# Optimization experiments

Measured on AMD Instinct MI355X. Metric: run time of the kernel, lower is better.

## Reference

```python
import jax, jax.numpy as jnp
import numpy as np

B, N, INP = 16, 1024, 256
HEADS, DIM_HEAD = 8, 32
INNER = HEADS * DIM_HEAD  # 256
OUP = 256
IH = IW = 32  # IH*IW == N


def _relative_index(ih, iw):
    # mirrors the torch __init__ construction (meshgrid indexing='ij')
    coords = np.stack(np.meshgrid(np.arange(ih), np.arange(iw), indexing='ij')).reshape(2, -1)
    rel = coords[:, :, None] - coords[:, None, :]  # [2, N, N]
    rel[0] += ih - 1
    rel[1] += iw - 1
    rel[0] *= 2 * iw - 1
    return rel.sum(0).reshape(-1)  # [N*N]


def setup_inputs() -> dict:
    key = jax.random.key(0)
    kx, kqkv, kout, kbias = jax.random.split(key, 4)
    x = jax.random.normal(kx, (B, N, INP), dtype=jnp.float32)
    w_qkv = jax.random.normal(kqkv, (INP, 3 * INNER), dtype=jnp.float32) * 0.02
    w_out = jax.random.normal(kout, (INNER, OUP), dtype=jnp.float32) * 0.02
    b_out = jnp.zeros((OUP,), dtype=jnp.float32)
    bias_table = jax.random.normal(kbias, ((2 * IH - 1) * (2 * IW - 1), HEADS), dtype=jnp.float32) * 0.02
    relative_index = jnp.asarray(_relative_index(IH, IW), dtype=jnp.int32)
    return {"x": x, "w_qkv": w_qkv, "w_out": w_out, "b_out": b_out,
            "bias_table": bias_table, "relative_index": relative_index}


def reference(x, w_qkv, w_out, b_out, bias_table, relative_index):
    b, n, _ = x.shape
    scale = DIM_HEAD ** (-0.5)
    qkv = x @ w_qkv  # [b, n, 3*inner]
    q, k, v = jnp.split(qkv, 3, axis=-1)
    split_heads = lambda t: t.reshape(b, n, HEADS, DIM_HEAD).transpose(0, 2, 1, 3)  # b h n d
    q, k, v = split_heads(q), split_heads(k), split_heads(v)
    dots = jnp.einsum('bhnd,bhmd->bhnm', q, k) * scale  # [b, h, n, n]
    # gather bias: (n*n, heads) -> (1, heads, n, n), matching '(h w) c -> 1 c h w'
    rel_bias = bias_table[relative_index].reshape(n, n, HEADS).transpose(2, 0, 1)[None]
    attn = jax.nn.softmax(dots + rel_bias, axis=-1)
    out = jnp.einsum('bhnm,bhmd->bhnd', attn, v)
    out = out.transpose(0, 2, 1, 3).reshape(b, n, INNER)  # b n (h d)
    return out @ w_out + b_out
```

## Files before the change

### kernel.cpp

```cpp
#include <hip/hip_runtime.h>
#include <hip/hip_bf16.h>

typedef __bf16 bf16;
typedef bf16 bf16x4 __attribute__((ext_vector_type(4)));
typedef bf16 bf16x8 __attribute__((ext_vector_type(8)));
typedef short s16x4 __attribute__((ext_vector_type(4)));
typedef float f32x4 __attribute__((ext_vector_type(4)));

#define MFMA32(A, B, C) __builtin_amdgcn_mfma_f32_16x16x32_bf16(A, B, C, 0, 0, 0)
#define MFMA16(A, B, C) __builtin_amdgcn_mfma_f32_16x16x16bf16_1k(A, B, C, 0, 0, 0)
#define GL2LDS16(gp, lp)                                                            \
  __builtin_amdgcn_global_load_lds((const __attribute__((address_space(1))) unsigned int*)(gp), \
                                   (__attribute__((address_space(3))) unsigned int*)(lp), 16, 0, 0)

static constexpr float SCALE = 0.17677669529663687f;
static constexpr float LOG2E = 1.4426950408889634f;

__global__ __launch_bounds__(256) void k_prep(const float* __restrict__ x,
                                              const float* __restrict__ wqkv,
                                              const float* __restrict__ wout,
                                              const float* __restrict__ table,
                                              const int* __restrict__ ridx,
                                              bf16* __restrict__ xb, bf16* __restrict__ wtq,
                                              bf16* __restrict__ wto, bf16* __restrict__ rbb) {
  const int tid = threadIdx.x;
  const int blk = blockIdx.x;
  if (blk < 2048) {
    int t = blk * 256 + tid;
    const float4* s = reinterpret_cast<const float4*>(x) + (size_t)t * 2;
    float4 a = s[0], c = s[1];
    bf16x8 o;
    o[0] = (bf16)a.x; o[1] = (bf16)a.y; o[2] = (bf16)a.z; o[3] = (bf16)a.w;
    o[4] = (bf16)c.x; o[5] = (bf16)c.y; o[6] = (bf16)c.z; o[7] = (bf16)c.w;
    reinterpret_cast<bf16x8*>(xb)[t] = o;
  } else if (blk < 3072) {
    int t = (blk - 2048) * 256 + tid;
    if (t < 196608) {
      int n = t >> 8, k = t & 255;
      wtq[t] = (bf16)wqkv[k * 768 + n];
    } else {
      int t2 = t - 196608;
      int n = t2 >> 8, k = t2 & 255;
      wto[t2] = (bf16)wout[k * 256 + n];
    }
  } else {
    const int bb2 = blk - 3072;
    const int qt = bb2 >> 6, kt = bb2 & 63;
    const int r = tid & 3, lane = tid >> 2;
    const int ln = lane & 15, quad = lane >> 4;
    const int qrow = qt * 16 + ln;
    const int key = kt * 16 + quad * 4 + r;
    const int idx = ridx[qrow * 1024 + key];
    const float4* p = reinterpret_cast<const float4*>(table) + idx * 2;
    float4 a = p[0], c = p[1];
    float vals[8] = {a.x, a.y, a.z, a.w, c.x, c.y, c.z, c.w};
    const int base = bb2 * 256 + tid;
#pragma unroll
    for (int h = 0; h < 8; ++h) rbb[h * 1048576 + base] = (bf16)(vals[h] * LOG2E);
  }
}

template <int EPI>
__global__ __launch_bounds__(256) void k_gemm(const bf16* __restrict__ A,
                                              const bf16* __restrict__ Bt,
                                              bf16* __restrict__ q, bf16* __restrict__ kk,
                                              bf16* __restrict__ vt, float* __restrict__ out,
                                              const float* __restrict__ bout) {
  __shared__ __align__(16) bf16 SM[16896];
  bf16(*As)[4096] = reinterpret_cast<bf16(*)[4096]>(SM);
  bf16(*Bs)[4096] = reinterpret_cast<bf16(*)[4096]>(SM + 8192);
  const int tid = threadIdx.x;
  const int ln = tid & 15, quad = (tid >> 4) & 3, wv = tid >> 6;
  const int wm = (wv >> 1) * 64, wn = (wv & 1) * 64;
  const int m0 = blockIdx.x * 128, n0 = blockIdx.y * 128;
  const int srow = tid >> 2, scg = (tid & 3) * 8;
  const bf16* ag = A + (size_t)(m0 + srow) * 256 + scg;
  const bf16* bg = Bt + (size_t)(n0 + srow) * 256 + scg;
  f32x4 acc[4][4] = {};

  GL2LDS16(ag, &As[0][tid * 8]);
  GL2LDS16(ag + 64 * 256, &As[0][2048 + tid * 8]);
  GL2LDS16(bg, &Bs[0][tid * 8]);
  GL2LDS16(bg + 64 * 256, &Bs[0][2048 + tid * 8]);

#pragma unroll 2
  for (int kt = 0; kt < 256; kt += 32) {
    const int cur = (kt >> 5) & 1, nxt = cur ^ 1;
    __syncthreads();
    if (kt < 224) {
      GL2LDS16(ag + kt + 32, &As[nxt][tid * 8]);
      GL2LDS16(ag + 64 * 256 + kt + 32, &As[nxt][2048 + tid * 8]);
      GL2LDS16(bg + kt + 32, &Bs[nxt][tid * 8]);
      GL2LDS16(bg + 64 * 256 + kt + 32, &Bs[nxt][2048 + tid * 8]);
    }
    bf16x8 af[4], bfr[4];
#pragma unroll
    for (int i = 0; i < 4; ++i)
      af[i] = *reinterpret_cast<const bf16x8*>(&As[cur][(wm + i * 16 + ln) * 32 + quad * 8]);
#pragma unroll
    for (int i = 0; i < 4; ++i)
      bfr[i] = *reinterpret_cast<const bf16x8*>(&Bs[cur][(wn + i * 16 + ln) * 32 + quad * 8]);
#pragma unroll
    for (int i = 0; i < 4; ++i)
#pragma unroll
      for (int j = 0; j < 4; ++j) acc[i][j] = MFMA32(af[i], bfr[j], acc[i][j]);
  }

  if (EPI == 0) {
    const int colbase = n0 + wn;
    const int seg = colbase >> 8;
    if (seg == 2) {
      __syncthreads();
#pragma unroll
      for (int i = 0; i < 4; ++i) {
#pragma unroll
        for (int j = 0; j < 4; ++j) {
          bf16x4 t;
#pragma unroll
          for (int r = 0; r < 4; ++r) t[r] = (bf16)acc[i][j][r];
          *reinterpret_cast<bf16x4*>(&SM[(wn + j * 16 + ln) * 132 + wm + i * 16 + quad * 4]) = t;
        }
      }
      __syncthreads();
      const int b = m0 >> 10;
      const int nbase = m0 & 1023;
      const int rc = tid & 15, c0 = tid >> 4;
      const int cb0 = n0 & 255;
#pragma unroll
      for (int p = 0; p < 8; ++p) {
        const int c = c0 + p * 16;
        const int gcol = cb0 + c;
        const int h = gcol >> 5, d = gcol & 31;
        bf16* dst = &vt[(b * 8 + h) * 32768 + d * 1024 + nbase + rc * 8];
        *reinterpret_cast<bf16x8*>(dst) =
            *reinterpret_cast<const bf16x8*>(&SM[c * 132 + rc * 8]);
      }
    } else {
      const int cb = colbase & 255;
      const float mul = (seg == 0) ? SCALE * LOG2E : 1.0f;
#pragma unroll
      for (int i = 0; i < 4; ++i) {
        const int gm = m0 + wm + i * 16 + quad * 4;
        const int b = gm >> 10;
#pragma unroll
        for (int j = 0; j < 4; ++j) {
          const int gc = cb + j * 16 + ln;
          const int h = gc >> 5, d = gc & 31;
#pragma unroll
          for (int r = 0; r < 4; ++r) {
            const int nseq = (gm + r) & 1023;
            bf16* dst = (seg == 0) ? q : kk;
            dst[(b * 8 + h) * 32768 + nseq * 32 + d] = (bf16)(acc[i][j][r] * mul);
          }
        }
      }
    }
  } else {
#pragma unroll
    for (int j = 0; j < 4; ++j) {
      const int gc = n0 + wn + j * 16 + ln;
      const float bb = bout[gc];
#pragma unroll
      for (int i = 0; i < 4; ++i) {
        const int gm = m0 + wm + i * 16 + quad * 4;
#pragma unroll
        for (int r = 0; r < 4; ++r) out[(size_t)(gm + r) * 256 + gc] = acc[i][j][r] + bb;
      }
    }
  }
}

__global__ __launch_bounds__(256, 4) void k_flash(const bf16* __restrict__ qs,
                                                  const bf16* __restrict__ ks,
                                                  const bf16* __restrict__ vtg,
                                                  const bf16* __restrict__ rbb,
                                                  bf16* __restrict__ ao) {
  __shared__ __align__(16) bf16 Ks[2][2048];
  __shared__ __align__(16) bf16 Vs[2][2048];
  const int tid = threadIdx.x;
  const int lane = tid & 63;
  const int ln = lane & 15, quad = lane >> 4, wv = tid >> 6;
  const int blk = blockIdx.x;
  const int bh = blk & 127;
  const int b = bh >> 3, h = bh & 7;
  const int qtw = (blk >> 7) * 4 + wv;
  const int q0 = qtw * 32;
  const bf16* qb = qs + bh * 32768;
  const bf16* kb = ks + bh * 32768;
  const bf16* vb = vtg + bh * 32768;
  const bf16* bbias0 = rbb + h * 1048576 + (2 * qtw) * 16384 + lane * 4;
  const bf16* bbias1 = bbias0 + 16384;

  const bf16* kg = kb + (tid >> 2) * 32 + (((tid & 3) ^ ((tid >> 3) & 3)) * 8);
  const bf16* vg = vb + (tid >> 3) * 1024 + (((tid & 7) ^ ((tid >> 3) & 7)) * 8);

  const bf16x8 qfrag0 = *reinterpret_cast<const bf16x8*>(&qb[(q0 + ln) * 32 + quad * 8]);
  const bf16x8 qfrag1 = *reinterpret_cast<const bf16x8*>(&qb[(q0 + 16 + ln) * 32 + quad * 8]);

  const int ksw = (quad ^ ((ln >> 1) & 3)) * 8;
  const int vswl = ln & 7;

  f32x4 a00 = {0.f, 0.f, 0.f, 0.f}, a01 = {0.f, 0.f, 0.f, 0.f};
  f32x4 a10 = {0.f, 0.f, 0.f, 0.f}, a11 = {0.f, 0.f, 0.f, 0.f};
  float lsum0 = 0.f, lsum1 = 0.f;

  bf16x4 cbf[2][2][4];
#pragma unroll
  for (int nt = 0; nt < 4; ++nt) {
    cbf[0][0][nt] = *reinterpret_cast<const bf16x4*>(&bbias0[nt * 256]);
    cbf[0][1][nt] = *reinterpret_cast<const bf16x4*>(&bbias1[nt * 256]);
  }
  GL2LDS16(kg, &Ks[0][tid * 8]);
  GL2LDS16(vg, &Vs[0][tid * 8]);

#pragma unroll 2
  for (int it = 0; it < 16; ++it) {
    const int cur = it & 1, nxt = cur ^ 1;
    const int k0 = it * 64;
    __syncthreads();
    if (it < 15) {
      GL2LDS16(kg + (k0 + 64) * 32, &Ks[nxt][tid * 8]);
      GL2LDS16(vg + k0 + 64, &Vs[nxt][tid * 8]);
#pragma unroll
      for (int nt = 0; nt < 4; ++nt) {
        cbf[nxt][0][nt] = *reinterpret_cast<const bf16x4*>(&bbias0[((it + 1) * 4 + nt) * 256]);
        cbf[nxt][1][nt] = *reinterpret_cast<const bf16x4*>(&bbias1[((it + 1) * 4 + nt) * 256]);
      }
    }
    bf16x8 kf[4];
#pragma unroll
    for (int nt = 0; nt < 4; ++nt)
      kf[nt] = *reinterpret_cast<const bf16x8*>(&Ks[cur][(nt * 16 + ln) * 32 + ksw]);
    s16x4 vfa[4], vfc[4];
#pragma unroll
    for (int nt = 0; nt < 4; ++nt) {
      const int col = ((2 * nt + (quad >> 1)) ^ vswl) * 8 + (quad & 1) * 4;
      vfa[nt] = *reinterpret_cast<const s16x4*>(&Vs[cur][ln * 64 + col]);
      vfc[nt] = *reinterpret_cast<const s16x4*>(&Vs[cur][(ln + 16) * 64 + col]);
    }
    f32x4 s0[4], s1[4];
#pragma unroll
    for (int nt = 0; nt < 4; ++nt) {
      f32x4 c0, c1;
#pragma unroll
      for (int e = 0; e < 4; ++e) {
        c0[e] = (float)cbf[cur][0][nt][e];
        c1[e] = (float)cbf[cur][1][nt][e];
      }
      s0[nt] = MFMA32(kf[nt], qfrag0, c0);
      s1[nt] = MFMA32(kf[nt], qfrag1, c1);
    }
    s16x4 p0[4], p1[4];
#pragma unroll
    for (int nt = 0; nt < 4; ++nt) {
      bf16x4 t0, t1;
#pragma unroll
      for (int e = 0; e < 4; ++e) {
        s0[nt][e] = __builtin_amdgcn_exp2f(s0[nt][e]);
        t0[e] = (bf16)s0[nt][e];
        s1[nt][e] = __builtin_amdgcn_exp2f(s1[nt][e]);
        t1[e] = (bf16)s1[nt][e];
      }
      lsum0 += (s0[nt][0] + s0[nt][1]) + (s0[nt][2] + s0[nt][3]);
      lsum1 += (s1[nt][0] + s1[nt][1]) + (s1[nt][2] + s1[nt][3]);
      p0[nt] = __builtin_bit_cast(s16x4, t0);
      p1[nt] = __builtin_bit_cast(s16x4, t1);
    }
#pragma unroll
    for (int nt = 0; nt < 4; ++nt) {
      a00 = MFMA16(p0[nt], vfa[nt], a00);
      a01 = MFMA16(p0[nt], vfc[nt], a01);
      a10 = MFMA16(p1[nt], vfa[nt], a10);
      a11 = MFMA16(p1[nt], vfc[nt], a11);
    }
  }
  __syncthreads();

  lsum0 += __shfl_xor(lsum0, 16, 64);
  lsum0 += __shfl_xor(lsum0, 32, 64);
  lsum1 += __shfl_xor(lsum1, 16, 64);
  lsum1 += __shfl_xor(lsum1, 32, 64);

#pragma unroll
  for (int r = 0; r < 4; ++r) {
    const float inv0 = __builtin_amdgcn_rcpf(__shfl(lsum0, quad * 4 + r, 64));
    const int row0 = q0 + quad * 4 + r;
    bf16* po0 = &ao[(size_t)(b * 1024 + row0) * 256 + h * 32 + ln];
    po0[0] = (bf16)(a00[r] * inv0);
    po0[16] = (bf16)(a01[r] * inv0);
    const float inv1 = __builtin_amdgcn_rcpf(__shfl(lsum1, quad * 4 + r, 64));
    const int row1 = q0 + 16 + quad * 4 + r;
    bf16* po1 = &ao[(size_t)(b * 1024 + row1) * 256 + h * 32 + ln];
    po1[0] = (bf16)(a10[r] * inv1);
    po1[16] = (bf16)(a11[r] * inv1);
  }
}

extern "C" void kernel_launch(void* const* d_in, const int* in_sizes, int n_in,
                              void* d_out, int out_size, void* d_ws, size_t ws_size,
                              hipStream_t stream) {
  const float* x = (const float*)d_in[0];
  const float* wqkv = (const float*)d_in[1];
  const float* wout = (const float*)d_in[2];
  const float* bout = (const float*)d_in[3];
  const float* btab = (const float*)d_in[4];
  const int* ridx = (const int*)d_in[5];
  float* out = (float*)d_out;

  char* ws = (char*)d_ws;
  bf16* xb  = (bf16*)(ws + 0);
  bf16* wtq = (bf16*)(ws + 8388608);
  bf16* wto = (bf16*)(ws + 8781824);
  bf16* q   = (bf16*)(ws + 8912896);
  bf16* k   = (bf16*)(ws + 17301504);
  bf16* vt  = (bf16*)(ws + 25690112);
  bf16* rb  = (bf16*)(ws + 34078720);
  bf16* ao  = (bf16*)(ws + 50855936);

  k_prep<<<7168, 256, 0, stream>>>(x, wqkv, wout, btab, ridx, xb, wtq, wto, rb);
  k_gemm<0><<<dim3(128, 6), 256, 0, stream>>>(xb, wtq, q, k, vt, nullptr, nullptr);
  k_flash<<<1024, 256, 0, stream>>>(q, k, vt, rb, ao);
  k_gemm<1><<<dim3(128, 2), 256, 0, stream>>>(ao, wto, nullptr, nullptr, nullptr, out, bout);
}
```

Before: 141.1 us.

## Move bias gather into QKV GEMM grid and compute row sums via MFMA

The relative-bias gather blocks move out of the prep kernel and become extra blocks in the QKV GEMM launch (grid y extended from 6 to 38), so the gather runs alongside the GEMM instead of delaying its start. In the flash kernel, the softmax denominator is now accumulated with an extra MFMA against a ones vector, replacing per-lane fp32 adds and the final cross-lane shuffles. The row sum is now taken over the bf16-rounded probabilities, which slightly changes numerics, and the flash kernel issues more MFMA work.

```diff
diff --git a/kernel.cpp b/kernel.cpp
--- a/kernel.cpp
+++ b/kernel.cpp
@@ -19,10 +19,8 @@
 __global__ __launch_bounds__(256) void k_prep(const float* __restrict__ x,
                                               const float* __restrict__ wqkv,
                                               const float* __restrict__ wout,
-                                              const float* __restrict__ table,
-                                              const int* __restrict__ ridx,
                                               bf16* __restrict__ xb, bf16* __restrict__ wtq,
-                                              bf16* __restrict__ wto, bf16* __restrict__ rbb) {
+                                              bf16* __restrict__ wto) {
   const int tid = threadIdx.x;
   const int blk = blockIdx.x;
   if (blk < 2048) {
@@ -33,7 +31,7 @@
     o[0] = (bf16)a.x; o[1] = (bf16)a.y; o[2] = (bf16)a.z; o[3] = (bf16)a.w;
     o[4] = (bf16)c.x; o[5] = (bf16)c.y; o[6] = (bf16)c.z; o[7] = (bf16)c.w;
     reinterpret_cast<bf16x8*>(xb)[t] = o;
-  } else if (blk < 3072) {
+  } else {
     int t = (blk - 2048) * 256 + tid;
     if (t < 196608) {
       int n = t >> 8, k = t & 255;
@@ -43,8 +41,22 @@
       int n = t2 >> 8, k = t2 & 255;
       wto[t2] = (bf16)wout[k * 256 + n];
     }
-  } else {
-    const int bb2 = blk - 3072;
+  }
+}
+
+template <int EPI>
+__global__ __launch_bounds__(256) void k_gemm(const bf16* __restrict__ A,
+                                              const bf16* __restrict__ Bt,
+                                              bf16* __restrict__ q, bf16* __restrict__ kk,
+                                              bf16* __restrict__ vt, float* __restrict__ out,
+                                              const float* __restrict__ bout,
+                                              const float* __restrict__ table,
+                                              const int* __restrict__ ridx,
+                                              bf16* __restrict__ rbb) {
+  __shared__ __align__(16) bf16 SM[16896];
+  const int tid = threadIdx.x;
+  if (EPI == 0 && blockIdx.y >= 6) {
+    const int bb2 = (blockIdx.y - 6) * 128 + blockIdx.x;
     const int qt = bb2 >> 6, kt = bb2 & 63;
     const int r = tid & 3, lane = tid >> 2;
     const int ln = lane & 15, quad = lane >> 4;
@@ -57,19 +69,10 @@
     const int base = bb2 * 256 + tid;
 #pragma unroll
     for (int h = 0; h < 8; ++h) rbb[h * 1048576 + base] = (bf16)(vals[h] * LOG2E);
-  }
-}
-
-template <int EPI>
-__global__ __launch_bounds__(256) void k_gemm(const bf16* __restrict__ A,
-                                              const bf16* __restrict__ Bt,
-                                              bf16* __restrict__ q, bf16* __restrict__ kk,
-                                              bf16* __restrict__ vt, float* __restrict__ out,
-                                              const float* __restrict__ bout) {
-  __shared__ __align__(16) bf16 SM[16896];
+    return;
+  }
   bf16(*As)[4096] = reinterpret_cast<bf16(*)[4096]>(SM);
   bf16(*Bs)[4096] = reinterpret_cast<bf16(*)[4096]>(SM + 8192);
-  const int tid = threadIdx.x;
   const int ln = tid & 15, quad = (tid >> 4) & 3, wv = tid >> 6;
   const int wm = (wv >> 1) * 64, wn = (wv & 1) * 64;
   const int m0 = blockIdx.x * 128, n0 = blockIdx.y * 128;
@@ -200,9 +203,11 @@
   const int ksw = (quad ^ ((ln >> 1) & 3)) * 8;
   const int vswl = ln & 7;
 
+  const s16x4 onesb = {(short)0x3F80, (short)0x3F80, (short)0x3F80, (short)0x3F80};
+
   f32x4 a00 = {0.f, 0.f, 0.f, 0.f}, a01 = {0.f, 0.f, 0.f, 0.f};
   f32x4 a10 = {0.f, 0.f, 0.f, 0.f}, a11 = {0.f, 0.f, 0.f, 0.f};
-  float lsum0 = 0.f, lsum1 = 0.f;
+  f32x4 ls0 = {0.f, 0.f, 0.f, 0.f}, ls1 = {0.f, 0.f, 0.f, 0.f};
 
   bf16x4 cbf[2][2][4];
 #pragma unroll
@@ -256,13 +261,9 @@
       bf16x4 t0, t1;
 #pragma unroll
       for (int e = 0; e < 4; ++e) {
-        s0[nt][e] = __builtin_amdgcn_exp2f(s0[nt][e]);
-        t0[e] = (bf16)s0[nt][e];
-        s1[nt][e] = __builtin_amdgcn_exp2f(s1[nt][e]);
-        t1[e] = (bf16)s1[nt][e];
-      }
-      lsum0 += (s0[nt][0] + s0[nt][1]) + (s0[nt][2] + s0[nt][3]);
-      lsum1 += (s1[nt][0] + s1[nt][1]) + (s1[nt][2] + s1[nt][3]);
+        t0[e] = (bf16)__builtin_amdgcn_exp2f(s0[nt][e]);
+        t1[e] = (bf16)__builtin_amdgcn_exp2f(s1[nt][e]);
+      }
       p0[nt] = __builtin_bit_cast(s16x4, t0);
       p1[nt] = __builtin_bit_cast(s16x4, t1);
     }
@@ -270,25 +271,22 @@
     for (int nt = 0; nt < 4; ++nt) {
       a00 = MFMA16(p0[nt], vfa[nt], a00);
       a01 = MFMA16(p0[nt], vfc[nt], a01);
+      ls0 = MFMA16(p0[nt], onesb, ls0);
       a10 = MFMA16(p1[nt], vfa[nt], a10);
       a11 = MFMA16(p1[nt], vfc[nt], a11);
+      ls1 = MFMA16(p1[nt], onesb, ls1);
     }
   }
   __syncthreads();
 
-  lsum0 += __shfl_xor(lsum0, 16, 64);
-  lsum0 += __shfl_xor(lsum0, 32, 64);
-  lsum1 += __shfl_xor(lsum1, 16, 64);
-  lsum1 += __shfl_xor(lsum1, 32, 64);
-
 #pragma unroll
   for (int r = 0; r < 4; ++r) {
-    const float inv0 = __builtin_amdgcn_rcpf(__shfl(lsum0, quad * 4 + r, 64));
+    const float inv0 = __builtin_amdgcn_rcpf(ls0[r]);
     const int row0 = q0 + quad * 4 + r;
     bf16* po0 = &ao[(size_t)(b * 1024 + row0) * 256 + h * 32 + ln];
     po0[0] = (bf16)(a00[r] * inv0);
     po0[16] = (bf16)(a01[r] * inv0);
-    const float inv1 = __builtin_amdgcn_rcpf(__shfl(lsum1, quad * 4 + r, 64));
+    const float inv1 = __builtin_amdgcn_rcpf(ls1[r]);
     const int row1 = q0 + 16 + quad * 4 + r;
     bf16* po1 = &ao[(size_t)(b * 1024 + row1) * 256 + h * 32 + ln];
     po1[0] = (bf16)(a10[r] * inv1);
@@ -317,8 +315,10 @@
   bf16* rb  = (bf16*)(ws + 34078720);
   bf16* ao  = (bf16*)(ws + 50855936);
 
-  k_prep<<<7168, 256, 0, stream>>>(x, wqkv, wout, btab, ridx, xb, wtq, wto, rb);
-  k_gemm<0><<<dim3(128, 6), 256, 0, stream>>>(xb, wtq, q, k, vt, nullptr, nullptr);
+  k_prep<<<3072, 256, 0, stream>>>(x, wqkv, wout, xb, wtq, wto);
+  k_gemm<0><<<dim3(128, 38), 256, 0, stream>>>(xb, wtq, q, k, vt, nullptr, nullptr,
+                                               btab, ridx, rb);
   k_flash<<<1024, 256, 0, stream>>>(q, k, vt, rb, ao);
-  k_gemm<1><<<dim3(128, 2), 256, 0, stream>>>(ao, wto, nullptr, nullptr, nullptr, out, bout);
+  k_gemm<1><<<dim3(128, 2), 256, 0, stream>>>(ao, wto, nullptr, nullptr, nullptr, out, bout,
+                                              nullptr, nullptr, nullptr);
 }
```

After: 145.3 us. 3.0% more time.
